# Performance work log

Hardware: AMD Instinct MI355X
Metric: run time of the kernel (lower is better)

Reference implementation:

```python
import jax, jax.numpy as jnp
import numpy as np

EPS = 1e-5

def _conv1x1(x, w, b):
    # x: [B, Cin, L], w: [Cout, Cin], b: [Cout]
    return jnp.einsum('oc,bcl->bol', w, x) + b[None, :, None]

def _bn(x, g, b):
    # BatchNorm1d in training mode: batch stats over (B, L), biased variance
    m = jnp.mean(x, axis=(0, 2), keepdims=True)
    v = jnp.var(x, axis=(0, 2), keepdims=True)
    return g[None, :, None] * (x - m) * jax.lax.rsqrt(v + EPS) + b[None, :, None]

def setup_inputs() -> dict:
    key = jax.random.key(0)
    ks = jax.random.split(key, 16)
    B, H, L, K = 32, 32, 32768, 7
    rel, im, out = H // 16, H // 8, H // 4          # 2, 4, 8
    cat = (1 + K) * rel                              # 16
    w = lambda k, shape: jax.random.normal(k, shape, jnp.float32) * 0.1
    return {
        'x': jax.random.normal(ks[0], (B, H, L), jnp.float32),
        'w_phi': w(ks[1], (rel, H)),  'b_phi': w(ks[2], (rel,)),
        'w_psi': w(ks[3], (rel, H)),  'b_psi': w(ks[4], (rel,)),
        'w_beta': w(ks[5], (out, H)), 'b_beta': w(ks[6], (out,)),
        'w_cw1': w(ks[7], (im, cat)), 'b_cw1': w(ks[8], (im,)),
        'w_cw2': w(ks[9], (out, im)), 'b_cw2': w(ks[10], (out,)),
        'w_out': w(ks[11], (H, out)), 'b_out': w(ks[12], (H,)),
        'g_cat': jnp.ones((cat,), jnp.float32),  'be_cat': jnp.zeros((cat,), jnp.float32),
        'g_im': jnp.ones((im,), jnp.float32),    'be_im': jnp.zeros((im,), jnp.float32),
        'g_aggr': jnp.ones((out,), jnp.float32), 'be_aggr': jnp.zeros((out,), jnp.float32),
        'g_hid': jnp.ones((H,), jnp.float32),    'be_hid': jnp.zeros((H,), jnp.float32),
        'kernel_size': 7,
    }

def reference(x, w_phi, b_phi, w_psi, b_psi, w_beta, b_beta,
              w_cw1, b_cw1, w_cw2, b_cw2, w_out, b_out,
              g_cat, be_cat, g_im, be_im, g_aggr, be_aggr, g_hid, be_hid,
              kernel_size):
    B, H, L = x.shape
    phi = _conv1x1(x, w_phi, b_phi)                       # [B, rel, L]
    psi = _conv1x1(x, w_psi, b_psi)                       # [B, rel, L]
    p = kernel_size // 2
    psi_pad = jnp.pad(psi, ((0, 0), (0, 0), (p, p)))
    # F.unfold with kernel (k,1): channel index = c*k + j -> stack kernel axis after channel
    psi_unf = jnp.stack([psi_pad[:, :, j:j + L] for j in range(kernel_size)], axis=2)
    psi_unf = psi_unf.reshape(B, psi.shape[1] * kernel_size, L)   # [B, rel*k, L]
    h = jnp.concatenate([phi, psi_unf], axis=1)           # [B, (1+k)*rel, L]
    h = jax.nn.relu(_bn(h, g_cat, be_cat))
    h = _conv1x1(h, w_cw1, b_cw1)
    h = jax.nn.relu(_bn(h, g_im, be_im))
    weight = _conv1x1(h, w_cw2, b_cw2)                    # [B, out, L]
    beta = _conv1x1(x, w_beta, b_beta)                    # [B, out, L]
    aggr = jax.nn.relu(_bn(weight * beta, g_aggr, be_aggr))
    y = x + _conv1x1(aggr, w_out, b_out)
    return jax.nn.relu(_bn(y, g_hid, be_hid))
```

## Files before the change

### kernel.cpp

```cpp
#include <hip/hip_runtime.h>
#include <math.h>

#define Bn 32
#define Hc 32
#define Ln 32768
#define RELC 2
#define IMC 4
#define OC 8
#define CATC 16
#define KS 7
#define NPOS (Bn*Ln)
#define TPB 256
#define VPT 4
#define PPB (TPB*VPT)
#define TILES (Ln/PPB)
#define NBLK (Bn*TILES)
#define NSLOT 16
#define SSTR 128

#define iS_PHI  0
#define iSS_PHI 2
#define iS_PSI  4
#define iSS_PSI 6
#define iS_T    8
#define iSS_T   12
#define iS_AP   16
#define iSS_AP  24
#define iS_Y    32
#define iSS_Y   64
#define bPF  0
#define bPFS 6
#define bQL  12
#define bQLS 18
#define NBST 24

#define FMA4(A,S,V) { A.x=fmaf((S),(V).x,A.x); A.y=fmaf((S),(V).y,A.y); A.z=fmaf((S),(V).z,A.z); A.w=fmaf((S),(V).w,A.w); }

__device__ inline float4 affrelu(float4 v, float a, float d){
    float4 r;
    r.x=fmaxf(fmaf(a,v.x,d),0.f); r.y=fmaxf(fmaf(a,v.y,d),0.f);
    r.z=fmaxf(fmaf(a,v.z,d),0.f); r.w=fmaxf(fmaf(a,v.w,d),0.f);
    return r;
}
__device__ inline double wredd(double v){
    #pragma unroll
    for (int o=32;o>0;o>>=1) v += __shfl_down(v,o,64);
    return v;
}
__device__ inline float wredf(float v){
    #pragma unroll
    for (int o=32;o>0;o>>=1) v += __shfl_down(v,o,64);
    return v;
}
__device__ inline void atomAddD(double* p, double v){ unsafeAtomicAdd(p, v); }

__device__ inline unsigned short f2b(float f){
    unsigned int u = __float_as_uint(f);
    u += 0x7FFFu + ((u>>16)&1u);
    return (unsigned short)(u>>16);
}
__device__ inline float b2f(unsigned short h){ return __uint_as_float(((unsigned int)h)<<16); }
__device__ inline ushort4 pack4r(float4 v, float4* r){
    ushort4 h;
    h.x=f2b(v.x); h.y=f2b(v.y); h.z=f2b(v.z); h.w=f2b(v.w);
    r->x=b2f(h.x); r->y=b2f(h.y); r->z=b2f(h.z); r->w=b2f(h.w);
    return h;
}
__device__ inline ushort4 pack4(float4 v){
    ushort4 h;
    h.x=f2b(v.x); h.y=f2b(v.y); h.z=f2b(v.z); h.w=f2b(v.w);
    return h;
}
__device__ inline float4 unpack4(ushort4 h){
    return make_float4(b2f(h.x),b2f(h.y),b2f(h.z),b2f(h.w));
}

__global__ void __launch_bounds__(TPB) k1(
    const float* __restrict__ x,
    const float* __restrict__ w_phi, const float* __restrict__ b_phi,
    const float* __restrict__ w_psi, const float* __restrict__ b_psi,
    const float* __restrict__ w_beta,const float* __restrict__ b_beta,
    unsigned short* __restrict__ phiB, unsigned short* __restrict__ psiB,
    unsigned short* __restrict__ betaB, unsigned short* __restrict__ xB,
    double* __restrict__ stats, double* __restrict__ bstats)
{
    __shared__ __align__(16) float wl[Hc*12 + 12];
    __shared__ double rbuf[4][8];
    const int tid = threadIdx.x;
    for (int i = tid; i < Hc*12; i += TPB) {
        int h = i/12, j = i%12;
        float v;
        if (j < 2)      v = w_phi[j*Hc + h];
        else if (j < 4) v = w_psi[(j-2)*Hc + h];
        else            v = w_beta[(j-4)*Hc + h];
        wl[h*12 + j] = v;
    }
    if (tid < 12)
        wl[Hc*12+tid] = (tid<2) ? b_phi[tid] : (tid<4) ? b_psi[tid-2] : b_beta[tid-4];
    __syncthreads();

    const int b    = blockIdx.x / TILES;
    const int tile = blockIdx.x % TILES;
    const int l0   = tile*PPB + tid*VPT;
    double* st = stats + (size_t)(blockIdx.x & (NSLOT-1))*SSTR;

    float4 acc[12];
    #pragma unroll
    for (int j=0;j<12;++j){ float bb = wl[Hc*12+j]; acc[j]=make_float4(bb,bb,bb,bb); }

    const float* xb = x + (size_t)b*Hc*Ln + l0;
    unsigned short* xw = xB + (size_t)b*Hc*Ln + l0;
    #pragma unroll 4
    for (int h=0; h<Hc; ++h) {
        const float4 xv = *(const float4*)(xb + (size_t)h*Ln);
        const float4 w0 = *(const float4*)(&wl[h*12+0]);
        const float4 w1 = *(const float4*)(&wl[h*12+4]);
        const float4 w2 = *(const float4*)(&wl[h*12+8]);
        FMA4(acc[0],w0.x,xv); FMA4(acc[1],w0.y,xv); FMA4(acc[2],w0.z,xv); FMA4(acc[3],w0.w,xv);
        FMA4(acc[4],w1.x,xv); FMA4(acc[5],w1.y,xv); FMA4(acc[6],w1.z,xv); FMA4(acc[7],w1.w,xv);
        FMA4(acc[8],w2.x,xv); FMA4(acc[9],w2.y,xv); FMA4(acc[10],w2.z,xv); FMA4(acc[11],w2.w,xv);
        *(ushort4*)(xw + (size_t)h*Ln) = pack4(xv);
    }
    float4 rphi[2], rpsi[2];
    #pragma unroll
    for (int c=0;c<RELC;++c){
        ushort4 hp = pack4r(acc[c], &rphi[c]);
        *(ushort4*)(phiB + ((size_t)(b*RELC+c))*Ln + l0) = hp;
        ushort4 hq = pack4r(acc[2+c], &rpsi[c]);
        *(ushort4*)(psiB + ((size_t)(b*RELC+c))*Ln + l0) = hq;
    }
    #pragma unroll
    for (int o=0;o<OC;++o)
        *(ushort4*)(betaB + ((size_t)(b*OC+o))*Ln + l0) = pack4(acc[4+o]);

    double vals[8];
    #pragma unroll
    for (int c=0;c<2;++c){
        float4 v = rphi[c];
        vals[c]   = (double)v.x+v.y+v.z+v.w;
        vals[2+c] = (double)v.x*v.x+(double)v.y*v.y+(double)v.z*v.z+(double)v.w*v.w;
        float4 u = rpsi[c];
        vals[4+c] = (double)u.x+u.y+u.z+u.w;
        vals[6+c] = (double)u.x*u.x+(double)u.y*u.y+(double)u.z*u.z+(double)u.w*u.w;
    }
    if (tile==0 || tile==TILES-1) {
        #pragma unroll
        for (int c=0;c<2;++c){
            const float pv[4] = {rpsi[c].x, rpsi[c].y, rpsi[c].z, rpsi[c].w};
            #pragma unroll
            for (int e=0;e<4;++e){
                int le = l0+e;
                if (le < 3) {
                    atomAddD(&bstats[bPF +c*3+le], (double)pv[e]);
                    atomAddD(&bstats[bPFS+c*3+le], (double)pv[e]*pv[e]);
                }
                if (le >= Ln-3) {
                    int i = le-(Ln-3);
                    atomAddD(&bstats[bQL +c*3+i], (double)pv[e]);
                    atomAddD(&bstats[bQLS+c*3+i], (double)pv[e]*pv[e]);
                }
            }
        }
    }
    const int lane=tid&63, wid=tid>>6;
    #pragma unroll
    for (int i=0;i<8;++i){ double r=wredd(vals[i]); if(lane==0) rbuf[wid][i]=r; }
    __syncthreads();
    if (tid<8) atomAddD(&st[iS_PHI+tid], rbuf[0][tid]+rbuf[1][tid]+rbuf[2][tid]+rbuf[3][tid]);
}

#define CAT_AFFINE(aCat,dCat)                                                              \
    if (tid < CATC){                                                                       \
        int ch=tid; double S=0,SS=0;                                                       \
        if (ch<2){                                                                         \
            for (int s=0;s<NSLOT;++s){ S+=stats[(size_t)s*SSTR+iS_PHI+ch]; SS+=stats[(size_t)s*SSTR+iSS_PHI+ch]; } \
        } else {                                                                           \
            int c=(ch-2)/KS, j=(ch-2)%KS, d=j-KS/2;                                        \
            for (int s=0;s<NSLOT;++s){ S+=stats[(size_t)s*SSTR+iS_PSI+c]; SS+=stats[(size_t)s*SSTR+iSS_PSI+c]; }   \
            if (d>0) for (int i=0;i<d;++i)   { S-=bstats[bPF+c*3+i];  SS-=bstats[bPFS+c*3+i]; } \
            if (d<0) for (int i=3+d;i<3;++i) { S-=bstats[bQL+c*3+i];  SS-=bstats[bQLS+c*3+i]; } \
        }                                                                                  \
        double m=S/N, v=SS/N-m*m, inv=1.0/sqrt(v+1e-5);                                    \
        aCat[ch]=(float)(g_cat[ch]*inv);                                                   \
        dCat[ch]=be_cat[ch]-(float)(m*inv*g_cat[ch]);                                      \
    }

#define IM_AG_AFFINE(aIm,dIm,aAg,dAg)                                                      \
    if (tid>=32 && tid<32+IMC){                                                            \
        int i=tid-32; double S=0,SS=0;                                                     \
        for (int s=0;s<NSLOT;++s){ S+=stats[(size_t)s*SSTR+iS_T+i]; SS+=stats[(size_t)s*SSTR+iSS_T+i]; } \
        double m=S/N, v=SS/N-m*m, inv=1.0/sqrt(v+1e-5);                                    \
        aIm[i]=(float)(g_im[i]*inv); dIm[i]=be_im[i]-(float)(m*inv*g_im[i]);               \
    }                                                                                      \
    if (tid>=48 && tid<48+OC){                                                             \
        int o=tid-48; double S=0,SS=0;                                                     \
        for (int s=0;s<NSLOT;++s){ S+=stats[(size_t)s*SSTR+iS_AP+o]; SS+=stats[(size_t)s*SSTR+iSS_AP+o]; } \
        double m=S/N, v=SS/N-m*m, inv=1.0/sqrt(v+1e-5);                                    \
        aAg[o]=(float)(g_ag[o]*inv); dAg[o]=be_ag[o]-(float)(m*inv*g_ag[o]);               \
    }

#define STAGE_PSI(psiT)                                                                    \
    _Pragma("unroll")                                                                      \
    for (int c=0;c<2;++c)                                                                  \
        for (int idx=tid; idx<1032; idx+=TPB) {                                            \
            int l = lb - 3 + idx;                                                          \
            psiT[c][idx] = (l>=0 && l<Ln && idx<1030) ? b2f(psiB[((size_t)(b*RELC+c))*Ln + l]) : 0.f; \
        }

#define COMPUTE_T(tacc,aCat,dCat,w1s,b1s,psiT)                                             \
    _Pragma("unroll")                                                                      \
    for (int o=0;o<IMC;++o){ float bb=b1s[o]; tacc[o]=make_float4(bb,bb,bb,bb); }          \
    _Pragma("unroll")                                                                      \
    for (int c=0;c<RELC;++c){                                                              \
        float4 pv = unpack4(*(const ushort4*)(phiB + ((size_t)(b*RELC+c))*Ln + lb + li));  \
        float4 hv = affrelu(pv, aCat[c], dCat[c]);                                         \
        _Pragma("unroll")                                                                  \
        for (int o=0;o<IMC;++o) FMA4(tacc[o], w1s[o*CATC+c], hv);                          \
    }                                                                                      \
    _Pragma("unroll")                                                                      \
    for (int c=0;c<RELC;++c){                                                              \
        float4 A  = *(const float4*)&psiT[c][li];                                          \
        float4 Bv = *(const float4*)&psiT[c][li+4];                                        \
        float4 Cv = *(const float4*)&psiT[c][li+8];                                        \
        float pr[12] = {A.x,A.y,A.z,A.w, Bv.x,Bv.y,Bv.z,Bv.w, Cv.x,Cv.y,Cv.z,Cv.w};        \
        _Pragma("unroll")                                                                  \
        for (int j=0;j<KS;++j){                                                            \
            int ch = 2 + c*KS + j;                                                         \
            float a=aCat[ch], d=dCat[ch];                                                  \
            float4 hv;                                                                     \
            hv.x=fmaxf(fmaf(a,pr[j+0],d),0.f);                                             \
            hv.y=fmaxf(fmaf(a,pr[j+1],d),0.f);                                             \
            hv.z=fmaxf(fmaf(a,pr[j+2],d),0.f);                                             \
            hv.w=fmaxf(fmaf(a,pr[j+3],d),0.f);                                             \
            _Pragma("unroll")                                                              \
            for (int o=0;o<IMC;++o) FMA4(tacc[o], w1s[o*CATC+ch], hv);                     \
        }                                                                                  \
    }

#define COMPUTE_AG(ag,tacc,aIm,dIm,aAg,dAg,w2s,b2s)                                        \
    {                                                                                      \
        float4 h2[IMC];                                                                    \
        _Pragma("unroll")                                                                  \
        for (int i=0;i<IMC;++i) h2[i]=affrelu(tacc[i],aIm[i],dIm[i]);                      \
        _Pragma("unroll")                                                                  \
        for (int o=0;o<OC;++o){                                                            \
            float bb=b2s[o];                                                               \
            float4 w=make_float4(bb,bb,bb,bb);                                             \
            _Pragma("unroll")                                                              \
            for (int i=0;i<IMC;++i) FMA4(w,w2s[o*IMC+i],h2[i]);                            \
            float4 bv = unpack4(*(const ushort4*)(betaB + ((size_t)(b*OC+o))*Ln + lb + li)); \
            float4 av; av.x=w.x*bv.x; av.y=w.y*bv.y; av.z=w.z*bv.z; av.w=w.w*bv.w;         \
            ag[o]=affrelu(av, aAg[o], dAg[o]);                                             \
        }                                                                                  \
    }

__global__ void __launch_bounds__(TPB) k3t(
    const unsigned short* __restrict__ phiB, const unsigned short* __restrict__ psiB,
    const float* __restrict__ w_cw1, const float* __restrict__ b_cw1,
    const float* __restrict__ g_cat, const float* __restrict__ be_cat,
    double* __restrict__ stats, const double* __restrict__ bstats)
{
    __shared__ float aCat[CATC], dCat[CATC];
    __shared__ float w1s[IMC*CATC], b1s[IMC];
    __shared__ __align__(16) float psiT[2][1032];
    __shared__ double rbuf[4][8];
    const int tid = threadIdx.x;
    const double N = (double)NPOS;
    const int b    = blockIdx.x / TILES;
    const int tile = blockIdx.x % TILES;
    const int lb   = tile*PPB;
    const int li   = tid*VPT;
    double* st = stats + (size_t)(blockIdx.x & (NSLOT-1))*SSTR;

    CAT_AFFINE(aCat,dCat)
    if (tid < IMC*CATC) w1s[tid] = w_cw1[tid];
    if (tid < IMC)      b1s[tid] = b_cw1[tid];
    STAGE_PSI(psiT)
    __syncthreads();

    float4 tacc[IMC];
    COMPUTE_T(tacc,aCat,dCat,w1s,b1s,psiT)

    double vals[8];
    #pragma unroll
    for (int o=0;o<IMC;++o){
        float4 v = tacc[o];
        vals[o]   = (double)v.x+v.y+v.z+v.w;
        vals[4+o] = (double)v.x*v.x+(double)v.y*v.y+(double)v.z*v.z+(double)v.w*v.w;
    }
    const int lane=tid&63, wid=tid>>6;
    #pragma unroll
    for (int i=0;i<8;++i){ double r=wredd(vals[i]); if(lane==0) rbuf[wid][i]=r; }
    __syncthreads();
    if (tid<8) atomAddD(&st[iS_T+tid], rbuf[0][tid]+rbuf[1][tid]+rbuf[2][tid]+rbuf[3][tid]);
}

__global__ void __launch_bounds__(TPB) k5a(
    const unsigned short* __restrict__ phiB, const unsigned short* __restrict__ psiB,
    const unsigned short* __restrict__ betaB,
    const float* __restrict__ w_cw1, const float* __restrict__ b_cw1,
    const float* __restrict__ w_cw2, const float* __restrict__ b_cw2,
    const float* __restrict__ g_cat, const float* __restrict__ be_cat,
    const float* __restrict__ g_im,  const float* __restrict__ be_im,
    double* __restrict__ stats, const double* __restrict__ bstats)
{
    __shared__ float aCat[CATC], dCat[CATC], aIm[IMC], dIm[IMC];
    __shared__ float w1s[IMC*CATC], b1s[IMC], w2s[OC*IMC], b2s[OC];
    __shared__ __align__(16) float psiT[2][1032];
    __shared__ double rbuf[4][16];
    const int tid = threadIdx.x;
    const double N = (double)NPOS;
    const int b    = blockIdx.x / TILES;
    const int tile = blockIdx.x % TILES;
    const int lb   = tile*PPB;
    const int li   = tid*VPT;
    double* st = stats + (size_t)(blockIdx.x & (NSLOT-1))*SSTR;

    CAT_AFFINE(aCat,dCat)
    if (tid>=32 && tid<32+IMC){
        int i=tid-32; double S=0,SS=0;
        for (int s=0;s<NSLOT;++s){ S+=stats[(size_t)s*SSTR+iS_T+i]; SS+=stats[(size_t)s*SSTR+iSS_T+i]; }
        double m=S/N, v=SS/N-m*m, inv=1.0/sqrt(v+1e-5);
        aIm[i]=(float)(g_im[i]*inv); dIm[i]=be_im[i]-(float)(m*inv*g_im[i]);
    }
    if (tid < IMC*CATC) w1s[tid] = w_cw1[tid];
    if (tid < IMC)      b1s[tid] = b_cw1[tid];
    if (tid>=64 && tid<64+OC*IMC) w2s[tid-64]=w_cw2[tid-64];
    if (tid>=96 && tid<96+OC)     b2s[tid-96]=b_cw2[tid-96];
    STAGE_PSI(psiT)
    __syncthreads();

    float4 tacc[IMC];
    COMPUTE_T(tacc,aCat,dCat,w1s,b1s,psiT)

    double vals[16];
    {
        float4 h2[IMC];
        #pragma unroll
        for (int i=0;i<IMC;++i) h2[i]=affrelu(tacc[i],aIm[i],dIm[i]);
        #pragma unroll
        for (int o=0;o<OC;++o){
            float bb=b2s[o];
            float4 w=make_float4(bb,bb,bb,bb);
            #pragma unroll
            for (int i=0;i<IMC;++i) FMA4(w,w2s[o*IMC+i],h2[i]);
            float4 bv = unpack4(*(const ushort4*)(betaB + ((size_t)(b*OC+o))*Ln + lb + li));
            float4 av; av.x=w.x*bv.x; av.y=w.y*bv.y; av.z=w.z*bv.z; av.w=w.w*bv.w;
            vals[o]   = (double)av.x+av.y+av.z+av.w;
            vals[8+o] = (double)av.x*av.x+(double)av.y*av.y+(double)av.z*av.z+(double)av.w*av.w;
        }
    }
    const int lane=tid&63, wid=tid>>6;
    #pragma unroll
    for (int i=0;i<16;++i){ double r=wredd(vals[i]); if(lane==0) rbuf[wid][i]=r; }
    __syncthreads();
    if (tid<16) atomAddD(&st[iS_AP+tid], rbuf[0][tid]+rbuf[1][tid]+rbuf[2][tid]+rbuf[3][tid]);
}

__global__ void __launch_bounds__(TPB) k7y(
    const unsigned short* __restrict__ xB,
    const unsigned short* __restrict__ phiB, const unsigned short* __restrict__ psiB,
    const unsigned short* __restrict__ betaB,
    const float* __restrict__ w_cw1, const float* __restrict__ b_cw1,
    const float* __restrict__ w_cw2, const float* __restrict__ b_cw2,
    const float* __restrict__ w_out, const float* __restrict__ b_out,
    const float* __restrict__ g_cat, const float* __restrict__ be_cat,
    const float* __restrict__ g_im,  const float* __restrict__ be_im,
    const float* __restrict__ g_ag,  const float* __restrict__ be_ag,
    double* __restrict__ stats, const double* __restrict__ bstats)
{
    __shared__ float aCat[CATC], dCat[CATC], aIm[IMC], dIm[IMC], aAg[OC], dAg[OC];
    __shared__ float w1s[IMC*CATC], b1s[IMC], w2s[OC*IMC], b2s[OC];
    __shared__ __align__(16) float wos[Hc*OC];
    __shared__ float bos[Hc];
    __shared__ __align__(16) float psiT[2][1032];
    __shared__ float fredS[Hc][4], fredQ[Hc][4];
    const int tid = threadIdx.x;
    const double N = (double)NPOS;
    const int b    = blockIdx.x / TILES;
    const int tile = blockIdx.x % TILES;
    const int lb   = tile*PPB;
    const int li   = tid*VPT;
    double* st = stats + (size_t)(blockIdx.x & (NSLOT-1))*SSTR;

    CAT_AFFINE(aCat,dCat)
    IM_AG_AFFINE(aIm,dIm,aAg,dAg)
    if (tid < IMC*CATC) w1s[tid] = w_cw1[tid];
    if (tid < IMC)      b1s[tid] = b_cw1[tid];
    if (tid>=64 && tid<64+OC*IMC) w2s[tid-64]=w_cw2[tid-64];
    if (tid>=96 && tid<96+OC)     b2s[tid-96]=b_cw2[tid-96];
    wos[tid] = w_out[tid];
    if (tid>=128 && tid<128+Hc) bos[tid-128]=b_out[tid-128];
    STAGE_PSI(psiT)
    __syncthreads();

    float4 tacc[IMC];
    COMPUTE_T(tacc,aCat,dCat,w1s,b1s,psiT)
    float4 ag[OC];
    COMPUTE_AG(ag,tacc,aIm,dIm,aAg,dAg,w2s,b2s)

    const int lane=tid&63, wid=tid>>6;
    const unsigned short* xb = xB + (size_t)b*Hc*Ln + lb + li;
    #pragma unroll 4
    for (int h=0;h<Hc;++h){
        float4 y = unpack4(*(const ushort4*)(xb + (size_t)h*Ln));
        float bb=bos[h]; y.x+=bb; y.y+=bb; y.z+=bb; y.w+=bb;
        #pragma unroll
        for (int o=0;o<OC;++o) FMA4(y, wos[h*OC+o], ag[o]);
        float fs=y.x+y.y+y.z+y.w;
        float fq=y.x*y.x+y.y*y.y+y.z*y.z+y.w*y.w;
        fs=wredf(fs); fq=wredf(fq);
        if (lane==0){ fredS[h][wid]=fs; fredQ[h][wid]=fq; }
    }
    __syncthreads();
    if (tid<Hc){
        double s=(double)fredS[tid][0]+fredS[tid][1]+fredS[tid][2]+fredS[tid][3];
        double q=(double)fredQ[tid][0]+fredQ[tid][1]+fredQ[tid][2]+fredQ[tid][3];
        atomAddD(&st[iS_Y +tid], s);
        atomAddD(&st[iSS_Y+tid], q);
    }
}

__global__ void __launch_bounds__(TPB) k9o(
    const unsigned short* __restrict__ xB,
    const unsigned short* __restrict__ phiB, const unsigned short* __restrict__ psiB,
    const unsigned short* __restrict__ betaB,
    const float* __restrict__ w_cw1, const float* __restrict__ b_cw1,
    const float* __restrict__ w_cw2, const float* __restrict__ b_cw2,
    const float* __restrict__ w_out, const float* __restrict__ b_out,
    const float* __restrict__ g_cat, const float* __restrict__ be_cat,
    const float* __restrict__ g_im,  const float* __restrict__ be_im,
    const float* __restrict__ g_ag,  const float* __restrict__ be_ag,
    const float* __restrict__ g_hid, const float* __restrict__ be_hid,
    float* __restrict__ out,
    const double* __restrict__ stats, const double* __restrict__ bstats)
{
    __shared__ float aCat[CATC], dCat[CATC], aIm[IMC], dIm[IMC], aAg[OC], dAg[OC];
    __shared__ float aHid[Hc], dHid[Hc];
    __shared__ float w1s[IMC*CATC], b1s[IMC], w2s[OC*IMC], b2s[OC];
    __shared__ __align__(16) float wos[Hc*OC];
    __shared__ float bos[Hc];
    __shared__ __align__(16) float psiT[2][1032];
    const int tid = threadIdx.x;
    const double N = (double)NPOS;
    const int b    = blockIdx.x / TILES;
    const int tile = blockIdx.x % TILES;
    const int lb   = tile*PPB;
    const int li   = tid*VPT;

    CAT_AFFINE(aCat,dCat)
    IM_AG_AFFINE(aIm,dIm,aAg,dAg)
    if (tid>=160 && tid<160+Hc){
        int h=tid-160; double S=0,SS=0;
        for (int s=0;s<NSLOT;++s){ S+=stats[(size_t)s*SSTR+iS_Y+h]; SS+=stats[(size_t)s*SSTR+iSS_Y+h]; }
        double m=S/N, v=SS/N-m*m, inv=1.0/sqrt(v+1e-5);
        aHid[h]=(float)(g_hid[h]*inv); dHid[h]=be_hid[h]-(float)(m*inv*g_hid[h]);
    }
    if (tid < IMC*CATC) w1s[tid] = w_cw1[tid];
    if (tid < IMC)      b1s[tid] = b_cw1[tid];
    if (tid>=64 && tid<64+OC*IMC) w2s[tid-64]=w_cw2[tid-64];
    if (tid>=96 && tid<96+OC)     b2s[tid-96]=b_cw2[tid-96];
    wos[tid] = w_out[tid];
    if (tid>=128 && tid<128+Hc) bos[tid-128]=b_out[tid-128];
    STAGE_PSI(psiT)
    __syncthreads();

    float4 tacc[IMC];
    COMPUTE_T(tacc,aCat,dCat,w1s,b1s,psiT)
    float4 ag[OC];
    COMPUTE_AG(ag,tacc,aIm,dIm,aAg,dAg,w2s,b2s)

    const unsigned short* xb = xB + (size_t)b*Hc*Ln + lb + li;
    float* ob = out + (size_t)b*Hc*Ln + lb + li;
    #pragma unroll 4
    for (int h=0;h<Hc;++h){
        float4 y = unpack4(*(const ushort4*)(xb + (size_t)h*Ln));
        float bb=bos[h]; y.x+=bb; y.y+=bb; y.z+=bb; y.w+=bb;
        #pragma unroll
        for (int o=0;o<OC;++o) FMA4(y, wos[h*OC+o], ag[o]);
        *(float4*)(ob + (size_t)h*Ln) = affrelu(y, aHid[h], dHid[h]);
    }
}

extern "C" void kernel_launch(void* const* d_in, const int* in_sizes, int n_in,
                              void* d_out, int out_size, void* d_ws, size_t ws_size,
                              hipStream_t stream)
{
    const float* x     =(const float*)d_in[0];
    const float* w_phi =(const float*)d_in[1];  const float* b_phi =(const float*)d_in[2];
    const float* w_psi =(const float*)d_in[3];  const float* b_psi =(const float*)d_in[4];
    const float* w_beta=(const float*)d_in[5];  const float* b_beta=(const float*)d_in[6];
    const float* w_cw1 =(const float*)d_in[7];  const float* b_cw1 =(const float*)d_in[8];
    const float* w_cw2 =(const float*)d_in[9];  const float* b_cw2 =(const float*)d_in[10];
    const float* w_out =(const float*)d_in[11]; const float* b_out =(const float*)d_in[12];
    const float* g_cat =(const float*)d_in[13]; const float* be_cat=(const float*)d_in[14];
    const float* g_im  =(const float*)d_in[15]; const float* be_im =(const float*)d_in[16];
    const float* g_ag  =(const float*)d_in[17]; const float* be_ag =(const float*)d_in[18];
    const float* g_hid =(const float*)d_in[19]; const float* be_hid=(const float*)d_in[20];

    double* stats  = (double*)d_ws;
    double* bstats = stats + (size_t)NSLOT*SSTR;
    unsigned short* base = (unsigned short*)((char*)d_ws + 32768);
    unsigned short* phiB  = base;
    unsigned short* psiB  = phiB  + (size_t)Bn*RELC*Ln;
    unsigned short* betaB = psiB  + (size_t)Bn*RELC*Ln;
    unsigned short* xB    = betaB + (size_t)Bn*OC*Ln;

    hipMemsetAsync(d_ws, 0, ((size_t)NSLOT*SSTR + NBST)*sizeof(double), stream);
    k1 <<<NBLK, TPB, 0, stream>>>(x, w_phi,b_phi, w_psi,b_psi, w_beta,b_beta,
                                  phiB,psiB,betaB,xB, stats,bstats);
    k3t<<<NBLK, TPB, 0, stream>>>(phiB,psiB, w_cw1,b_cw1, g_cat,be_cat, stats,bstats);
    k5a<<<NBLK, TPB, 0, stream>>>(phiB,psiB,betaB, w_cw1,b_cw1, w_cw2,b_cw2,
                                  g_cat,be_cat, g_im,be_im, stats,bstats);
    k7y<<<NBLK, TPB, 0, stream>>>(xB, phiB,psiB,betaB, w_cw1,b_cw1, w_cw2,b_cw2, w_out,b_out,
                                  g_cat,be_cat, g_im,be_im, g_ag,be_ag, stats,bstats);
    k9o<<<NBLK, TPB, 0, stream>>>(xB, phiB,psiB,betaB, w_cw1,b_cw1, w_cw2,b_cw2, w_out,b_out,
                                  g_cat,be_cat, g_im,be_im, g_ag,be_ag, g_hid,be_hid,
                                  (float*)d_out, stats,bstats);
}
```

Measured before the change: 195.0 us.

## Split bf16 conversion of x into its own kernel and vectorize psi staging

```diff
diff --git a/kernel.cpp b/kernel.cpp
--- a/kernel.cpp
+++ b/kernel.cpp
@@ -17,6 +17,7 @@
 #define NBLK (Bn*TILES)
 #define NSLOT 16
 #define SSTR 128
+#define NELEM4 ((size_t)Bn*Hc*Ln/4)
 
 #define iS_PHI  0
 #define iSS_PHI 2
@@ -74,14 +75,25 @@
 __device__ inline float4 unpack4(ushort4 h){
     return make_float4(b2f(h.x),b2f(h.y),b2f(h.z),b2f(h.w));
 }
+typedef unsigned short us8 __attribute__((ext_vector_type(8)));
+
+__global__ void __launch_bounds__(TPB) k0(const float* __restrict__ x, unsigned short* __restrict__ xB)
+{
+    size_t i = (size_t)blockIdx.x*TPB + threadIdx.x;
+    const size_t stride = (size_t)gridDim.x*TPB;
+    for (; i < NELEM4; i += stride){
+        float4 v = ((const float4*)x)[i];
+        ((ushort4*)xB)[i] = pack4(v);
+    }
+}
 
 __global__ void __launch_bounds__(TPB) k1(
-    const float* __restrict__ x,
+    const unsigned short* __restrict__ xB,
     const float* __restrict__ w_phi, const float* __restrict__ b_phi,
     const float* __restrict__ w_psi, const float* __restrict__ b_psi,
     const float* __restrict__ w_beta,const float* __restrict__ b_beta,
     unsigned short* __restrict__ phiB, unsigned short* __restrict__ psiB,
-    unsigned short* __restrict__ betaB, unsigned short* __restrict__ xB,
+    unsigned short* __restrict__ betaB,
     double* __restrict__ stats, double* __restrict__ bstats)
 {
     __shared__ __align__(16) float wl[Hc*12 + 12];
@@ -108,18 +120,16 @@
     #pragma unroll
     for (int j=0;j<12;++j){ float bb = wl[Hc*12+j]; acc[j]=make_float4(bb,bb,bb,bb); }
 
-    const float* xb = x + (size_t)b*Hc*Ln + l0;
-    unsigned short* xw = xB + (size_t)b*Hc*Ln + l0;
-    #pragma unroll 4
+    const unsigned short* xb = xB + (size_t)b*Hc*Ln + l0;
+    #pragma unroll 8
     for (int h=0; h<Hc; ++h) {
-        const float4 xv = *(const float4*)(xb + (size_t)h*Ln);
+        const float4 xv = unpack4(*(const ushort4*)(xb + (size_t)h*Ln));
         const float4 w0 = *(const float4*)(&wl[h*12+0]);
         const float4 w1 = *(const float4*)(&wl[h*12+4]);
         const float4 w2 = *(const float4*)(&wl[h*12+8]);
         FMA4(acc[0],w0.x,xv); FMA4(acc[1],w0.y,xv); FMA4(acc[2],w0.z,xv); FMA4(acc[3],w0.w,xv);
         FMA4(acc[4],w1.x,xv); FMA4(acc[5],w1.y,xv); FMA4(acc[6],w1.z,xv); FMA4(acc[7],w1.w,xv);
         FMA4(acc[8],w2.x,xv); FMA4(acc[9],w2.y,xv); FMA4(acc[10],w2.z,xv); FMA4(acc[11],w2.w,xv);
-        *(ushort4*)(xw + (size_t)h*Ln) = pack4(xv);
     }
     float4 rphi[2], rpsi[2];
     #pragma unroll
@@ -199,13 +209,17 @@
         aAg[o]=(float)(g_ag[o]*inv); dAg[o]=be_ag[o]-(float)(m*inv*g_ag[o]);               \
     }
 
-#define STAGE_PSI(psiT)                                                                    \
-    _Pragma("unroll")                                                                      \
-    for (int c=0;c<2;++c)                                                                  \
-        for (int idx=tid; idx<1032; idx+=TPB) {                                            \
-            int l = lb - 3 + idx;                                                          \
-            psiT[c][idx] = (l>=0 && l<Ln && idx<1030) ? b2f(psiB[((size_t)(b*RELC+c))*Ln + l]) : 0.f; \
-        }
+#define STAGE_PSI_V(psiT)                                                                  \
+    {                                                                                      \
+        int c_ = tid >> 7, k_ = tid & 127;                                                 \
+        us8 v_ = *(const us8*)(psiB + ((size_t)(b*RELC+c_))*Ln + lb + 8*k_);               \
+        _Pragma("unroll")                                                                  \
+        for (int j_=0;j_<8;++j_) psiT[c_][3+8*k_+j_] = b2f(v_[j_]);                        \
+        if (tid < 6){ int cc=tid/3, ii=tid%3;                                              \
+            psiT[cc][ii] = (tile>0) ? b2f(psiB[((size_t)(b*RELC+cc))*Ln + lb-3+ii]) : 0.f; }\
+        else if (tid < 12){ int kk=tid-6, cc=kk/3, ii=kk%3;                                \
+            psiT[cc][1027+ii] = (tile<TILES-1) ? b2f(psiB[((size_t)(b*RELC+cc))*Ln + lb+1024+ii]) : 0.f; } \
+    }
 
 #define COMPUTE_T(tacc,aCat,dCat,w1s,b1s,psiT)                                             \
     _Pragma("unroll")                                                                      \
@@ -275,7 +289,7 @@
     CAT_AFFINE(aCat,dCat)
     if (tid < IMC*CATC) w1s[tid] = w_cw1[tid];
     if (tid < IMC)      b1s[tid] = b_cw1[tid];
-    STAGE_PSI(psiT)
+    STAGE_PSI_V(psiT)
     __syncthreads();
 
     float4 tacc[IMC];
@@ -327,7 +341,7 @@
     if (tid < IMC)      b1s[tid] = b_cw1[tid];
     if (tid>=64 && tid<64+OC*IMC) w2s[tid-64]=w_cw2[tid-64];
     if (tid>=96 && tid<96+OC)     b2s[tid-96]=b_cw2[tid-96];
-    STAGE_PSI(psiT)
+    STAGE_PSI_V(psiT)
     __syncthreads();
 
     float4 tacc[IMC];
@@ -391,7 +405,7 @@
     if (tid>=96 && tid<96+OC)     b2s[tid-96]=b_cw2[tid-96];
     wos[tid] = w_out[tid];
     if (tid>=128 && tid<128+Hc) bos[tid-128]=b_out[tid-128];
-    STAGE_PSI(psiT)
+    STAGE_PSI_V(psiT)
     __syncthreads();
 
     float4 tacc[IMC];
@@ -401,7 +415,7 @@
 
     const int lane=tid&63, wid=tid>>6;
     const unsigned short* xb = xB + (size_t)b*Hc*Ln + lb + li;
-    #pragma unroll 4
+    #pragma unroll 8
     for (int h=0;h<Hc;++h){
         float4 y = unpack4(*(const ushort4*)(xb + (size_t)h*Ln));
         float bb=bos[h]; y.x+=bb; y.y+=bb; y.z+=bb; y.w+=bb;
@@ -462,7 +476,7 @@
     if (tid>=96 && tid<96+OC)     b2s[tid-96]=b_cw2[tid-96];
     wos[tid] = w_out[tid];
     if (tid>=128 && tid<128+Hc) bos[tid-128]=b_out[tid-128];
-    STAGE_PSI(psiT)
+    STAGE_PSI_V(psiT)
     __syncthreads();
 
     float4 tacc[IMC];
@@ -472,7 +486,7 @@
 
     const unsigned short* xb = xB + (size_t)b*Hc*Ln + lb + li;
     float* ob = out + (size_t)b*Hc*Ln + lb + li;
-    #pragma unroll 4
+    #pragma unroll 8
     for (int h=0;h<Hc;++h){
         float4 y = unpack4(*(const ushort4*)(xb + (size_t)h*Ln));
         float bb=bos[h]; y.x+=bb; y.y+=bb; y.z+=bb; y.w+=bb;
@@ -507,8 +521,9 @@
     unsigned short* xB    = betaB + (size_t)Bn*OC*Ln;
 
     hipMemsetAsync(d_ws, 0, ((size_t)NSLOT*SSTR + NBST)*sizeof(double), stream);
-    k1 <<<NBLK, TPB, 0, stream>>>(x, w_phi,b_phi, w_psi,b_psi, w_beta,b_beta,
-                                  phiB,psiB,betaB,xB, stats,bstats);
+    k0 <<<2048, TPB, 0, stream>>>(x, xB);
+    k1 <<<NBLK, TPB, 0, stream>>>(xB, w_phi,b_phi, w_psi,b_psi, w_beta,b_beta,
+                                  phiB,psiB,betaB, stats,bstats);
     k3t<<<NBLK, TPB, 0, stream>>>(phiB,psiB, w_cw1,b_cw1, g_cat,be_cat, stats,bstats);
     k5a<<<NBLK, TPB, 0, stream>>>(phiB,psiB,betaB, w_cw1,b_cw1, w_cw2,b_cw2,
                                   g_cat,be_cat, g_im,be_im, stats,bstats);
```

After: 197.4 us. About the same (+1.3%).
